# Performance work log

Hardware: AMD Instinct MI355X
Metric: run time of the kernel (lower is better)

The kernel has to match this reference:

```python
import jax, jax.numpy as jnp
import numpy as np

ROBOT_W = 1.0
PHASE_W = 1.0
COHER_W = 10.0
SPEED_W = 5.0
MAX_SPEED = 10.0
SMOOTH_VEL_W = 0.05
SMOOTH_ACC_W = 0.01

# illegal phase transitions {(0,2),(1,0),(2,0),(2,1)} as a 3x3 lookup table
_ILLEGAL = np.zeros((3, 3), dtype=bool)
for a, b in [(0, 2), (1, 0), (2, 0), (2, 1)]:
    _ILLEGAL[a, b] = True
ILLEGAL_TABLE = jnp.asarray(_ILLEGAL)


def setup_inputs() -> dict:
    key = jax.random.key(0)
    k1, k2, k3, k4 = jax.random.split(key, 4)
    B, T = 256, 8192
    # scale by 8 so per-frame speeds (norm of diffs of 3-vectors) exceed MAX_SPEED
    pred_robot = jax.random.normal(k1, (B, T, 12), dtype=jnp.float32) * 8.0
    gt_robot = jax.random.normal(k2, (B, T, 12), dtype=jnp.float32) * 8.0
    pred_phase = jax.random.normal(k3, (B, T, 3), dtype=jnp.float32)
    gt_phase = jax.random.randint(k4, (B, T), 0, 3, dtype=jnp.int32)
    return {"pred_robot": pred_robot, "pred_phase": pred_phase,
            "gt_robot": gt_robot, "gt_phase": gt_phase}


def _coherence_loss(phase_logits):
    # vectorized replacement for the O(B*T) Python double loop
    p = jnp.argmax(phase_logits, axis=-1)            # [B, T]
    pt, pt1 = p[:, :-1], p[:, 1:]                    # [B, T-1]
    illegal = ILLEGAL_TABLE[pt, pt1]                 # [B, T-1] bool
    # logit of the (illegal) predicted phase at t+1
    sel = jnp.take_along_axis(phase_logits[:, 1:], pt1[..., None], axis=-1)[..., 0]
    loss_sum = jnp.sum(jnp.where(illegal, sel * sel, 0.0))
    count = jnp.sum(illegal)
    return jnp.where(count > 0, loss_sum / jnp.maximum(count, 1).astype(sel.dtype), 0.0)


def _speed_loss(pred_robot):
    B, T, D = pred_robot.shape
    vel = pred_robot[:, 1:] - pred_robot[:, :-1]     # [B, T-1, 12]
    pts = vel.reshape(B, T - 1, 4, 3)
    speeds = jnp.linalg.norm(pts, axis=-1)           # [B, T-1, 4]
    pen = jax.nn.relu(speeds - MAX_SPEED)
    return SPEED_W * jnp.mean(pen * pen)


def reference(pred_robot, pred_phase, gt_robot, gt_phase):
    # MSE over robot trajectory
    robot_loss = jnp.mean((pred_robot - gt_robot) ** 2)
    # cross-entropy over 3 phase classes
    logp = jax.nn.log_softmax(pred_phase, axis=-1)   # [B, T, 3]
    nll = -jnp.take_along_axis(logp, gt_phase[..., None].astype(jnp.int32), axis=-1)[..., 0]
    phase_loss = jnp.mean(nll)
    coherence = _coherence_loss(pred_phase)
    speed_loss = _speed_loss(pred_robot)
    vel = pred_robot[:, 1:] - pred_robot[:, :-1]
    vel_loss = jnp.mean(vel * vel)
    acc = pred_robot[:, 2:] - 2.0 * pred_robot[:, 1:-1] + pred_robot[:, :-2]
    acc_loss = jnp.mean(acc * acc)
    total = (ROBOT_W * robot_loss + PHASE_W * phase_loss + COHER_W * coherence
             + speed_loss + SMOOTH_VEL_W * vel_loss + SMOOTH_ACC_W * acc_loss)
    return total
```

## Files before the change

### kernel.cpp

```cpp
#include <hip/hip_runtime.h>
#include <math.h>

#define B_DIM 256
#define T_DIM 8192
#define BLOCK 256
#define NSLOT 256
#define NBLK  1024
#define ROWS_TOT (B_DIM * T_DIM)
#define NTILES (ROWS_TOT / BLOCK)
#define NT_PER (NTILES / NBLK)
#define NF4  (ROWS_TOT * 3)
#define NPH4 (ROWS_TOT * 3 / 4)


struct Stage {
    float4 A0, A1, A2;
    float4 G0, G1, G2;
    float4 At;
    float4 Ph;
    int    gph;
};

__device__ __forceinline__ Stage load_tile(int tile, int tid,
    const float4* __restrict__ pred4, const float4* __restrict__ gt4,
    const float4* __restrict__ ph4,   const int* __restrict__ gtp)
{
    Stage st;
    const int R = tile * BLOCK;
    const size_t b4 = (size_t)R * 3;

    st.A0 = pred4[b4 + tid];        st.G0 = gt4[b4 + tid];
    st.A1 = pred4[b4 + tid + 256];  st.G1 = gt4[b4 + tid + 256];
    st.A2 = pred4[b4 + tid + 512];  st.G2 = gt4[b4 + tid + 512];

    if (tid < 6) {
        size_t it4 = b4 + 768 + tid;
        if (it4 > (size_t)(NF4 - 1)) it4 = (size_t)(NF4 - 1);
        st.At = pred4[it4];
    } else {
        st.At = make_float4(0.f, 0.f, 0.f, 0.f);
    }

    const size_t p4 = (size_t)192 * tile;
    const int phcnt = (p4 + 193 <= (size_t)NPH4) ? 193 : 192;
    st.Ph = (tid < phcnt) ? ph4[p4 + tid] : make_float4(0.f, 0.f, 0.f, 0.f);

    st.gph = gtp[R + tid];
    return st;
}

__device__ __forceinline__ float pen_term(float s) {
    float d = fmaxf(sqrtf(s) - 10.0f, 0.0f);
    return d * d;
}
__device__ __forceinline__ void argmax3(float l0, float l1, float l2, int &p, float &m) {
    p = 0; m = l0;
    if (l1 > m) { m = l1; p = 1; }
    if (l2 > m) { m = l2; p = 2; }
}
__device__ __forceinline__ float nll3(float l0, float l1, float l2, int g) {
    float mx = fmaxf(l0, fmaxf(l1, l2));
    float s = __expf(l0 - mx) + __expf(l1 - mx) + __expf(l2 - mx);
    float sel = (g == 0) ? l0 : ((g == 1) ? l1 : l2);
    return mx + __logf(s) - sel;
}

__global__ __launch_bounds__(BLOCK) void combined_loss_main(
    const float4* __restrict__ pred4,
    const float4* __restrict__ ph4,
    const float4* __restrict__ gt4,
    const int*    __restrict__ gt_phase,
    double* __restrict__ ws)
{
    __shared__ float4 s_pred[774];
    __shared__ float4 s_ph4[194];
    __shared__ float  s_red[4][6];
    const float* s_ph = (const float*)s_ph4;

    const int tid = threadIdx.x;
    const int blk = blockIdx.x;

    float sse = 0.f, nll = 0.f, csum = 0.f, ccnt = 0.f;
    float pen2 = 0.f, velsq = 0.f, accsq = 0.f;

    Stage cur = load_tile(blk, tid, pred4, gt4, ph4, gt_phase);

    for (int it = 0; it < NT_PER; ++it) {
        const int tile = it * NBLK + blk;

        __syncthreads();
        s_pred[tid]       = cur.A0;
        s_pred[tid + 256] = cur.A1;
        s_pred[tid + 512] = cur.A2;
        if (tid < 6)   s_pred[768 + tid] = cur.At;
        if (tid < 193) s_ph4[tid] = cur.Ph;
        {
            float d;
            d = cur.A0.x - cur.G0.x; sse = fmaf(d, d, sse);
            d = cur.A0.y - cur.G0.y; sse = fmaf(d, d, sse);
            d = cur.A0.z - cur.G0.z; sse = fmaf(d, d, sse);
            d = cur.A0.w - cur.G0.w; sse = fmaf(d, d, sse);
            d = cur.A1.x - cur.G1.x; sse = fmaf(d, d, sse);
            d = cur.A1.y - cur.G1.y; sse = fmaf(d, d, sse);
            d = cur.A1.z - cur.G1.z; sse = fmaf(d, d, sse);
            d = cur.A1.w - cur.G1.w; sse = fmaf(d, d, sse);
            d = cur.A2.x - cur.G2.x; sse = fmaf(d, d, sse);
            d = cur.A2.y - cur.G2.y; sse = fmaf(d, d, sse);
            d = cur.A2.z - cur.G2.z; sse = fmaf(d, d, sse);
            d = cur.A2.w - cur.G2.w; sse = fmaf(d, d, sse);
        }
        const int gph = cur.gph;
        __syncthreads();

        Stage nxt;
        if (it + 1 < NT_PER) nxt = load_tile((it + 1) * NBLK + blk, tid, pred4, gt4, ph4, gt_phase);
        else                 nxt = cur;

        const int t  = (tile * BLOCK + tid) & (T_DIM - 1);
        const bool v1 = t < (T_DIM - 1);
        const bool v2 = t < (T_DIM - 2);
        const int l3 = 3 * tid;

        const float4 r0a = s_pred[l3],     r0b = s_pred[l3 + 1], r0c = s_pred[l3 + 2];
        const float4 r1a = s_pred[l3 + 3], r1b = s_pred[l3 + 4], r1c = s_pred[l3 + 5];
        const float4 r2a = s_pred[l3 + 6], r2b = s_pred[l3 + 7], r2c = s_pred[l3 + 8];

        {
            const float v0 = r1a.x - r0a.x, v1f = r1a.y - r0a.y, v2f = r1a.z - r0a.z, v3 = r1a.w - r0a.w;
            const float v4 = r1b.x - r0b.x, v5  = r1b.y - r0b.y, v6  = r1b.z - r0b.z, v7 = r1b.w - r0b.w;
            const float v8 = r1c.x - r0c.x, v9  = r1c.y - r0c.y, v10 = r1c.z - r0c.z, v11 = r1c.w - r0c.w;
            const float q0 = v0*v0, q1 = v1f*v1f, q2 = v2f*v2f, q3 = v3*v3;
            const float q4 = v4*v4, q5 = v5*v5,   q6 = v6*v6,   q7 = v7*v7;
            const float q8 = v8*v8, q9 = v9*v9,   q10 = v10*v10, q11 = v11*v11;
            if (v1) {
                velsq += (q0+q1+q2+q3) + (q4+q5+q6+q7) + (q8+q9+q10+q11);
                pen2  += pen_term(q0+q1+q2) + pen_term(q3+q4+q5)
                       + pen_term(q6+q7+q8) + pen_term(q9+q10+q11);
            }
        }
        if (v2) {
            float a;
            a = r2a.x - 2.0f*r1a.x + r0a.x; accsq = fmaf(a, a, accsq);
            a = r2a.y - 2.0f*r1a.y + r0a.y; accsq = fmaf(a, a, accsq);
            a = r2a.z - 2.0f*r1a.z + r0a.z; accsq = fmaf(a, a, accsq);
            a = r2a.w - 2.0f*r1a.w + r0a.w; accsq = fmaf(a, a, accsq);
            a = r2b.x - 2.0f*r1b.x + r0b.x; accsq = fmaf(a, a, accsq);
            a = r2b.y - 2.0f*r1b.y + r0b.y; accsq = fmaf(a, a, accsq);
            a = r2b.z - 2.0f*r1b.z + r0b.z; accsq = fmaf(a, a, accsq);
            a = r2b.w - 2.0f*r1b.w + r0b.w; accsq = fmaf(a, a, accsq);
            a = r2c.x - 2.0f*r1c.x + r0c.x; accsq = fmaf(a, a, accsq);
            a = r2c.y - 2.0f*r1c.y + r0c.y; accsq = fmaf(a, a, accsq);
            a = r2c.z - 2.0f*r1c.z + r0c.z; accsq = fmaf(a, a, accsq);
            a = r2c.w - 2.0f*r1c.w + r0c.w; accsq = fmaf(a, a, accsq);
        }
        {
            const float p00 = s_ph[l3], p01 = s_ph[l3 + 1], p02 = s_ph[l3 + 2];
            nll += nll3(p00, p01, p02, gph);
            if (v1) {
                const float p10 = s_ph[l3 + 3], p11 = s_ph[l3 + 4], p12 = s_ph[l3 + 5];
                int pP, pN; float mP, mN;
                argmax3(p00, p01, p02, pP, mP);
                argmax3(p10, p11, p12, pN, mN);
                const int mask = (pP == 0) ? 4 : ((pP == 1) ? 1 : 3);
                if ((mask >> pN) & 1) { csum += mN * mN; ccnt += 1.f; }
            }
        }

        cur = nxt;
    }

    float vals[6] = { fmaf(12.0f, nll, sse), csum, ccnt, pen2, velsq, accsq };
    #pragma unroll
    for (int off = 32; off > 0; off >>= 1) {
        #pragma unroll
        for (int q = 0; q < 6; ++q)
            vals[q] += __shfl_down(vals[q], off, 64);
    }
    const int wave = tid >> 6, lane = tid & 63;
    if (lane == 0) {
        #pragma unroll
        for (int q = 0; q < 6; ++q) s_red[wave][q] = vals[q];
    }
    __syncthreads();
    if (tid < 6) {
        const double acc = (double)s_red[0][tid] + (double)s_red[1][tid]
                         + (double)s_red[2][tid] + (double)s_red[3][tid];
        atomicAdd(&ws[(size_t)(blk & (NSLOT - 1)) * 8 + tid], acc);
    }
}

__global__ __launch_bounds__(256) void combined_loss_final(
    const double* __restrict__ ws, float* __restrict__ out)
{
    __shared__ double sred[4][6];
    const int tid = threadIdx.x;
    double v[6];
    #pragma unroll
    for (int q = 0; q < 6; ++q) v[q] = ws[(size_t)tid * 8 + q];
    #pragma unroll
    for (int off = 32; off > 0; off >>= 1) {
        #pragma unroll
        for (int q = 0; q < 6; ++q)
            v[q] += __shfl_down(v[q], off, 64);
    }
    const int wave = tid >> 6, lane = tid & 63;
    if (lane == 0) {
        #pragma unroll
        for (int q = 0; q < 6; ++q) sred[wave][q] = v[q];
    }
    __syncthreads();
    if (tid == 0) {
        double s[6];
        #pragma unroll
        for (int q = 0; q < 6; ++q)
            s[q] = sred[0][q] + sred[1][q] + sred[2][q] + sred[3][q];
        const double robot_phase = s[0] / (double)((size_t)B_DIM * T_DIM * 12);
        const double coher = (s[2] > 0.0) ? (s[1] / fmax(s[2], 1.0)) : 0.0;
        const double speed = 5.0  * (s[3] / (double)((size_t)B_DIM * (T_DIM - 1) * 4));
        const double vel   = 0.05 * (s[4] / (double)((size_t)B_DIM * (T_DIM - 1) * 12));
        const double acc   = 0.01 * (s[5] / (double)((size_t)B_DIM * (T_DIM - 2) * 12));
        out[0] = (float)(robot_phase + 10.0 * coher + speed + vel + acc);
    }
}

extern "C" void kernel_launch(void* const* d_in, const int* in_sizes, int n_in,
                              void* d_out, int out_size, void* d_ws, size_t ws_size,
                              hipStream_t stream)
{
    const float4* pred4      = (const float4*)d_in[0];
    const float4* ph4        = (const float4*)d_in[1];
    const float4* gt4        = (const float4*)d_in[2];
    const int*    gt_phase   = (const int*)d_in[3];
    double* ws  = (double*)d_ws;
    float*  out = (float*)d_out;

    hipMemsetAsync(d_ws, 0, (size_t)NSLOT * 8 * sizeof(double), stream);

    combined_loss_main<<<dim3(NBLK), BLOCK, 0, stream>>>(pred4, ph4, gt4, gt_phase, ws);
    combined_loss_final<<<1, 256, 0, stream>>>(ws, out);
}
```

Baseline: 244.2 us.

## Replace LDS tile staging with direct per-thread row-pair global loads

Drops the shared-memory staging and double-buffered tile loads. Each thread now handles a pair of consecutive rows, reading neighbour rows straight from global memory (through cache) for velocity and acceleration. The phase loss moves to a second loop with float2/int2 loads. This removes LDS traffic and block barriers, but each thread's float4 loads are strided by 96 bytes across lanes (less coalesced) and predicted rows are fetched twice.

```diff
diff --git a/kernel.cpp b/kernel.cpp
--- a/kernel.cpp
+++ b/kernel.cpp
@@ -4,50 +4,14 @@
 #define B_DIM 256
 #define T_DIM 8192
 #define BLOCK 256
+#define GRID  1024
 #define NSLOT 256
-#define NBLK  1024
 #define ROWS_TOT (B_DIM * T_DIM)
-#define NTILES (ROWS_TOT / BLOCK)
-#define NT_PER (NTILES / NBLK)
-#define NF4  (ROWS_TOT * 3)
-#define NPH4 (ROWS_TOT * 3 / 4)
-
-
-struct Stage {
-    float4 A0, A1, A2;
-    float4 G0, G1, G2;
-    float4 At;
-    float4 Ph;
-    int    gph;
-};
-
-__device__ __forceinline__ Stage load_tile(int tile, int tid,
-    const float4* __restrict__ pred4, const float4* __restrict__ gt4,
-    const float4* __restrict__ ph4,   const int* __restrict__ gtp)
-{
-    Stage st;
-    const int R = tile * BLOCK;
-    const size_t b4 = (size_t)R * 3;
-
-    st.A0 = pred4[b4 + tid];        st.G0 = gt4[b4 + tid];
-    st.A1 = pred4[b4 + tid + 256];  st.G1 = gt4[b4 + tid + 256];
-    st.A2 = pred4[b4 + tid + 512];  st.G2 = gt4[b4 + tid + 512];
-
-    if (tid < 6) {
-        size_t it4 = b4 + 768 + tid;
-        if (it4 > (size_t)(NF4 - 1)) it4 = (size_t)(NF4 - 1);
-        st.At = pred4[it4];
-    } else {
-        st.At = make_float4(0.f, 0.f, 0.f, 0.f);
-    }
-
-    const size_t p4 = (size_t)192 * tile;
-    const int phcnt = (p4 + 193 <= (size_t)NPH4) ? 193 : 192;
-    st.Ph = (tid < phcnt) ? ph4[p4 + tid] : make_float4(0.f, 0.f, 0.f, 0.f);
-
-    st.gph = gtp[R + tid];
-    return st;
-}
+#define NPAIR (ROWS_TOT / 2)
+#define NT    (GRID * BLOCK)
+#define NITER (NPAIR / NT)
+#define NF4   (ROWS_TOT * 3)
+
 
 __device__ __forceinline__ float pen_term(float s) {
     float d = fmaxf(sqrtf(s) - 10.0f, 0.0f);
@@ -64,112 +28,113 @@
     float sel = (g == 0) ? l0 : ((g == 1) ? l1 : l2);
     return mx + __logf(s) - sel;
 }
-
-__global__ __launch_bounds__(BLOCK) void combined_loss_main(
+__device__ __forceinline__ void sse4(const float4 &a, const float4 &g, float &s) {
+    float d;
+    d = a.x - g.x; s = fmaf(d, d, s);  d = a.y - g.y; s = fmaf(d, d, s);
+    d = a.z - g.z; s = fmaf(d, d, s);  d = a.w - g.w; s = fmaf(d, d, s);
+}
+__device__ __forceinline__ void vel12(const float4 &p0a, const float4 &p0b, const float4 &p0c,
+                                      const float4 &p1a, const float4 &p1b, const float4 &p1c,
+                                      float &velsq, float &pen2) {
+    float t;
+    t = p1a.x - p0a.x; const float q0  = t * t;
+    t = p1a.y - p0a.y; const float q1  = t * t;
+    t = p1a.z - p0a.z; const float q2  = t * t;
+    t = p1a.w - p0a.w; const float q3  = t * t;
+    t = p1b.x - p0b.x; const float q4  = t * t;
+    t = p1b.y - p0b.y; const float q5  = t * t;
+    t = p1b.z - p0b.z; const float q6  = t * t;
+    t = p1b.w - p0b.w; const float q7  = t * t;
+    t = p1c.x - p0c.x; const float q8  = t * t;
+    t = p1c.y - p0c.y; const float q9  = t * t;
+    t = p1c.z - p0c.z; const float q10 = t * t;
+    t = p1c.w - p0c.w; const float q11 = t * t;
+    velsq += (q0 + q1 + q2 + q3) + (q4 + q5 + q6 + q7) + (q8 + q9 + q10 + q11);
+    pen2  += pen_term(q0 + q1 + q2) + pen_term(q3 + q4 + q5)
+           + pen_term(q6 + q7 + q8) + pen_term(q9 + q10 + q11);
+}
+__device__ __forceinline__ void acc4(const float4 &r0, const float4 &r1, const float4 &r2, float &accsq) {
+    float a;
+    a = r2.x - 2.0f * r1.x + r0.x; accsq = fmaf(a, a, accsq);
+    a = r2.y - 2.0f * r1.y + r0.y; accsq = fmaf(a, a, accsq);
+    a = r2.z - 2.0f * r1.z + r0.z; accsq = fmaf(a, a, accsq);
+    a = r2.w - 2.0f * r1.w + r0.w; accsq = fmaf(a, a, accsq);
+}
+
+__global__ __launch_bounds__(BLOCK, 4) void combined_loss_main(
     const float4* __restrict__ pred4,
-    const float4* __restrict__ ph4,
+    const float*  __restrict__ ph,
     const float4* __restrict__ gt4,
     const int*    __restrict__ gt_phase,
     double* __restrict__ ws)
 {
-    __shared__ float4 s_pred[774];
-    __shared__ float4 s_ph4[194];
-    __shared__ float  s_red[4][6];
-    const float* s_ph = (const float*)s_ph4;
-
-    const int tid = threadIdx.x;
-    const int blk = blockIdx.x;
-
-    float sse = 0.f, nll = 0.f, csum = 0.f, ccnt = 0.f;
+    __shared__ float s_red[4][6];
+    const int tid  = threadIdx.x;
+    const int blk  = blockIdx.x;
+    const int gtid = blk * BLOCK + tid;
+
+    float sse = 0.f, nllv = 0.f, csum = 0.f, ccnt = 0.f;
     float pen2 = 0.f, velsq = 0.f, accsq = 0.f;
 
-    Stage cur = load_tile(blk, tid, pred4, gt4, ph4, gt_phase);
-
-    for (int it = 0; it < NT_PER; ++it) {
-        const int tile = it * NBLK + blk;
-
-        __syncthreads();
-        s_pred[tid]       = cur.A0;
-        s_pred[tid + 256] = cur.A1;
-        s_pred[tid + 512] = cur.A2;
-        if (tid < 6)   s_pred[768 + tid] = cur.At;
-        if (tid < 193) s_ph4[tid] = cur.Ph;
-        {
-            float d;
-            d = cur.A0.x - cur.G0.x; sse = fmaf(d, d, sse);
-            d = cur.A0.y - cur.G0.y; sse = fmaf(d, d, sse);
-            d = cur.A0.z - cur.G0.z; sse = fmaf(d, d, sse);
-            d = cur.A0.w - cur.G0.w; sse = fmaf(d, d, sse);
-            d = cur.A1.x - cur.G1.x; sse = fmaf(d, d, sse);
-            d = cur.A1.y - cur.G1.y; sse = fmaf(d, d, sse);
-            d = cur.A1.z - cur.G1.z; sse = fmaf(d, d, sse);
-            d = cur.A1.w - cur.G1.w; sse = fmaf(d, d, sse);
-            d = cur.A2.x - cur.G2.x; sse = fmaf(d, d, sse);
-            d = cur.A2.y - cur.G2.y; sse = fmaf(d, d, sse);
-            d = cur.A2.z - cur.G2.z; sse = fmaf(d, d, sse);
-            d = cur.A2.w - cur.G2.w; sse = fmaf(d, d, sse);
+    #pragma unroll 1
+    for (int u = 0; u < NITER; ++u) {
+        const int P = u * NT + gtid;
+        const bool tail = ((P + 1) & 4095) == 0;
+        const size_t fp = (size_t)P * 6;
+        const size_t ep = tail ? fp : fp + 6;
+
+        const float4 A0 = pred4[fp + 0], A1 = pred4[fp + 1], A2 = pred4[fp + 2];
+        const float4 A3 = pred4[fp + 3], A4 = pred4[fp + 4], A5 = pred4[fp + 5];
+        const float4 G0 = gt4[fp + 0],   G1 = gt4[fp + 1],   G2 = gt4[fp + 2];
+        const float4 G3 = gt4[fp + 3],   G4 = gt4[fp + 4],   G5 = gt4[fp + 5];
+        const float4 E0 = pred4[ep + 0], E1 = pred4[ep + 1], E2 = pred4[ep + 2];
+        const float4 E3 = pred4[ep + 3], E4 = pred4[ep + 4], E5 = pred4[ep + 5];
+
+        sse4(A0, G0, sse); sse4(A1, G1, sse); sse4(A2, G2, sse);
+        sse4(A3, G3, sse); sse4(A4, G4, sse); sse4(A5, G5, sse);
+
+        vel12(A0, A1, A2, A3, A4, A5, velsq, pen2);
+        if (!tail) {
+            vel12(A3, A4, A5, E0, E1, E2, velsq, pen2);
+            acc4(A0, A3, E0, accsq);
+            acc4(A1, A4, E1, accsq);
+            acc4(A2, A5, E2, accsq);
+            acc4(A3, E0, E3, accsq);
+            acc4(A4, E1, E4, accsq);
+            acc4(A5, E2, E5, accsq);
         }
-        const int gph = cur.gph;
-        __syncthreads();
-
-        Stage nxt;
-        if (it + 1 < NT_PER) nxt = load_tile((it + 1) * NBLK + blk, tid, pred4, gt4, ph4, gt_phase);
-        else                 nxt = cur;
-
-        const int t  = (tile * BLOCK + tid) & (T_DIM - 1);
-        const bool v1 = t < (T_DIM - 1);
-        const bool v2 = t < (T_DIM - 2);
-        const int l3 = 3 * tid;
-
-        const float4 r0a = s_pred[l3],     r0b = s_pred[l3 + 1], r0c = s_pred[l3 + 2];
-        const float4 r1a = s_pred[l3 + 3], r1b = s_pred[l3 + 4], r1c = s_pred[l3 + 5];
-        const float4 r2a = s_pred[l3 + 6], r2b = s_pred[l3 + 7], r2c = s_pred[l3 + 8];
-
-        {
-            const float v0 = r1a.x - r0a.x, v1f = r1a.y - r0a.y, v2f = r1a.z - r0a.z, v3 = r1a.w - r0a.w;
-            const float v4 = r1b.x - r0b.x, v5  = r1b.y - r0b.y, v6  = r1b.z - r0b.z, v7 = r1b.w - r0b.w;
-            const float v8 = r1c.x - r0c.x, v9  = r1c.y - r0c.y, v10 = r1c.z - r0c.z, v11 = r1c.w - r0c.w;
-            const float q0 = v0*v0, q1 = v1f*v1f, q2 = v2f*v2f, q3 = v3*v3;
-            const float q4 = v4*v4, q5 = v5*v5,   q6 = v6*v6,   q7 = v7*v7;
-            const float q8 = v8*v8, q9 = v9*v9,   q10 = v10*v10, q11 = v11*v11;
-            if (v1) {
-                velsq += (q0+q1+q2+q3) + (q4+q5+q6+q7) + (q8+q9+q10+q11);
-                pen2  += pen_term(q0+q1+q2) + pen_term(q3+q4+q5)
-                       + pen_term(q6+q7+q8) + pen_term(q9+q10+q11);
-            }
+    }
+
+    const float2* ph2  = (const float2*)ph;
+    const int2*   gtp2 = (const int2*)gt_phase;
+    #pragma unroll 1
+    for (int u = 0; u < NITER; ++u) {
+        const int L = u * NT + gtid;
+        const bool tail = ((L + 1) & 4095) == 0;
+        const size_t pb = (size_t)L * 3;
+        const size_t qb = tail ? pb : pb + 3;
+
+        const float2 a  = ph2[pb + 0], b = ph2[pb + 1], c = ph2[pb + 2];
+        const float2 e0 = ph2[qb + 0], e1 = ph2[qb + 1];
+        const int2   gg = gtp2[L];
+
+        nllv += nll3(a.x, a.y, b.x, gg.x);
+        nllv += nll3(b.y, c.x, c.y, gg.y);
+
+        int p0, p1, p2; float m0, m1, m2;
+        argmax3(a.x,  a.y,  b.x,  p0, m0);
+        argmax3(b.y,  c.x,  c.y,  p1, m1);
+        argmax3(e0.x, e0.y, e1.x, p2, m2);
+
+        const int mask0 = (p0 == 0) ? 4 : ((p0 == 1) ? 1 : 3);
+        if ((mask0 >> p1) & 1) { csum += m1 * m1; ccnt += 1.f; }
+        if (!tail) {
+            const int mask1 = (p1 == 0) ? 4 : ((p1 == 1) ? 1 : 3);
+            if ((mask1 >> p2) & 1) { csum += m2 * m2; ccnt += 1.f; }
         }
-        if (v2) {
-            float a;
-            a = r2a.x - 2.0f*r1a.x + r0a.x; accsq = fmaf(a, a, accsq);
-            a = r2a.y - 2.0f*r1a.y + r0a.y; accsq = fmaf(a, a, accsq);
-            a = r2a.z - 2.0f*r1a.z + r0a.z; accsq = fmaf(a, a, accsq);
-            a = r2a.w - 2.0f*r1a.w + r0a.w; accsq = fmaf(a, a, accsq);
-            a = r2b.x - 2.0f*r1b.x + r0b.x; accsq = fmaf(a, a, accsq);
-            a = r2b.y - 2.0f*r1b.y + r0b.y; accsq = fmaf(a, a, accsq);
-            a = r2b.z - 2.0f*r1b.z + r0b.z; accsq = fmaf(a, a, accsq);
-            a = r2b.w - 2.0f*r1b.w + r0b.w; accsq = fmaf(a, a, accsq);
-            a = r2c.x - 2.0f*r1c.x + r0c.x; accsq = fmaf(a, a, accsq);
-            a = r2c.y - 2.0f*r1c.y + r0c.y; accsq = fmaf(a, a, accsq);
-            a = r2c.z - 2.0f*r1c.z + r0c.z; accsq = fmaf(a, a, accsq);
-            a = r2c.w - 2.0f*r1c.w + r0c.w; accsq = fmaf(a, a, accsq);
-        }
-        {
-            const float p00 = s_ph[l3], p01 = s_ph[l3 + 1], p02 = s_ph[l3 + 2];
-            nll += nll3(p00, p01, p02, gph);
-            if (v1) {
-                const float p10 = s_ph[l3 + 3], p11 = s_ph[l3 + 4], p12 = s_ph[l3 + 5];
-                int pP, pN; float mP, mN;
-                argmax3(p00, p01, p02, pP, mP);
-                argmax3(p10, p11, p12, pN, mN);
-                const int mask = (pP == 0) ? 4 : ((pP == 1) ? 1 : 3);
-                if ((mask >> pN) & 1) { csum += mN * mN; ccnt += 1.f; }
-            }
-        }
-
-        cur = nxt;
-    }
-
-    float vals[6] = { fmaf(12.0f, nll, sse), csum, ccnt, pen2, velsq, accsq };
+    }
+
+    float vals[6] = { fmaf(12.0f, nllv, sse), csum, ccnt, pen2, velsq, accsq };
     #pragma unroll
     for (int off = 32; off > 0; off >>= 1) {
         #pragma unroll
@@ -228,7 +193,7 @@
                               hipStream_t stream)
 {
     const float4* pred4      = (const float4*)d_in[0];
-    const float4* ph4        = (const float4*)d_in[1];
+    const float*  pred_phase = (const float*)d_in[1];
     const float4* gt4        = (const float4*)d_in[2];
     const int*    gt_phase   = (const int*)d_in[3];
     double* ws  = (double*)d_ws;
@@ -236,6 +201,6 @@
 
     hipMemsetAsync(d_ws, 0, (size_t)NSLOT * 8 * sizeof(double), stream);
 
-    combined_loss_main<<<dim3(NBLK), BLOCK, 0, stream>>>(pred4, ph4, gt4, gt_phase, ws);
+    combined_loss_main<<<dim3(GRID), BLOCK, 0, stream>>>(pred4, pred_phase, gt4, gt_phase, ws);
     combined_loss_final<<<1, 256, 0, stream>>>(ws, out);
 }
```

New measurement: 243.5 us. Within noise of the previous version (-0.3%).
